# Kernel optimization log

Hardware: AMD Instinct MI355X
Metric: run time of the kernel (lower is better)

Reference implementation:

```python
import jax, jax.numpy as jnp
import numpy as np

VOCAB = 10000
HID = 256
BATCH = 32
STEPS = 256


def setup_inputs() -> dict:
    key = jax.random.key(0)
    k1, k2, k3, k4 = jax.random.split(key, 4)
    # glorot-uniform style scaling
    s_xh = np.sqrt(6.0 / (VOCAB + HID)).astype(np.float32)
    s_hh = np.sqrt(6.0 / (HID + HID)).astype(np.float32)
    s_d = np.sqrt(6.0 / (HID + VOCAB)).astype(np.float32)
    return {
        "tokens": jax.random.randint(k1, (BATCH, STEPS), 0, VOCAB, dtype=jnp.int32),
        "W_xh": jax.random.uniform(k2, (VOCAB, HID), jnp.float32, -s_xh, s_xh),
        "W_hh": jax.random.uniform(k3, (HID, HID), jnp.float32, -s_hh, s_hh),
        "b_h": jnp.zeros((HID,), jnp.float32),
        "W_d": jax.random.uniform(k4, (HID, VOCAB), jnp.float32, -s_d, s_d),
        "b_d": jnp.zeros((VOCAB,), jnp.float32),
        "h0": jnp.zeros((BATCH, HID), jnp.float32),
    }


def reference(tokens, W_xh, W_hh, b_h, W_d, b_d, h0):
    # call(): X = one_hot(transpose(tokens), vocab)  -> time-major [T, B, V]
    # one_hot(x) @ W_xh is exactly a row gather from W_xh (same math, efficient form)
    xw = W_xh[jnp.transpose(tokens)]  # [T, B, H]

    # SimpleRNNCell: h_t = tanh(x_t @ W_xh + h_{t-1} @ W_hh + b)
    def step(h, xt):
        h_new = jnp.tanh(xt + h @ W_hh + b_h)
        return h_new, h_new

    state, Y = jax.lax.scan(step, h0, xw)  # Y: [T, B, H], state: [B, H]

    # Dense over flattened sequence outputs -> [T*B, vocab]
    output = Y.reshape(-1, Y.shape[-1]) @ W_d + b_d
    return output, state
```

## Files before the change

kernel.cpp:

```cpp
#include <hip/hip_runtime.h>
#include <hip/hip_bf16.h>

#define VOCAB 10000
#define HID 256
#define BATCH 32
#define STEPS 256
#define MROWS (STEPS * BATCH)

typedef __bf16 bf16x8 __attribute__((ext_vector_type(8)));
typedef float f32x4 __attribute__((ext_vector_type(4)));

__global__ void transpose_wd_kernel(const float* __restrict__ Wd,
                                    __hip_bfloat16* __restrict__ WdT) {
    __shared__ __hip_bfloat16 tile[64][68];
    const int n0 = blockIdx.x * 64;
    const int k0 = blockIdx.y * 64;
    const int tid = threadIdx.x;
    const int lane = tid & 63;
    const int w = tid >> 6;

#pragma unroll
    for (int i = 0; i < 16; ++i) {
        int k = w * 16 + i;
        int n = lane;
        float v = (n0 + n < VOCAB) ? Wd[(size_t)(k0 + k) * VOCAB + n0 + n] : 0.f;
        tile[n][k] = __float2bfloat16(v);
    }
    __syncthreads();
#pragma unroll
    for (int i = 0; i < 16; ++i) {
        int n = w * 16 + i;
        int k = lane;
        if (n0 + n < VOCAB)
            WdT[(size_t)(n0 + n) * HID + k0 + k] = tile[n][k];
    }
}

#define HHALF 132

__global__ __launch_bounds__(512)
__attribute__((amdgpu_waves_per_eu(2, 2)))
void rnn_kernel(const int* __restrict__ tokens, const float* __restrict__ Wxh,
                const float* __restrict__ Whh, const float* __restrict__ bh,
                const float* __restrict__ h0, __hip_bfloat16* __restrict__ ybf,
                float* __restrict__ state_out) {
    const int b = blockIdx.x;
    const int tid = threadIdx.x;
    const int j = tid >> 1;
    const int q = tid & 1;

    __shared__ alignas(16) float hbuf[2][2][HHALF];

    float w[128];
#pragma unroll
    for (int i = 0; i < 128; ++i)
        w[i] = Whh[(size_t)(q * 128 + i) * HID + j];
#pragma unroll
    for (int i = 0; i < 128; ++i)
        asm volatile("" : "+v"(w[i]));

    if (q == 0) hbuf[0][j >> 7][j & 127] = h0[b * HID + j];
    const float bj = bh[j];
    const int* trow = tokens + b * STEPS;

    float x = Wxh[(size_t)trow[0] * HID + j];
    __syncthreads();

    float hn = 0.f;
    int cur = 0;
    for (int t = 0; t < STEPS; ++t) {
        int tn = (t + 1 < STEPS) ? t + 1 : t;
        float xn = Wxh[(size_t)trow[tn] * HID + j];

        const float* hrow = &hbuf[cur][q][0];
        float a0 = 0.f, a1 = 0.f, a2 = 0.f, a3 = 0.f;
#pragma unroll
        for (int i4 = 0; i4 < 32; ++i4) {
            float4 hv = *reinterpret_cast<const float4*>(&hrow[i4 * 4]);
            a0 += hv.x * w[i4 * 4 + 0];
            a1 += hv.y * w[i4 * 4 + 1];
            a2 += hv.z * w[i4 * 4 + 2];
            a3 += hv.w * w[i4 * 4 + 3];
        }
        float partial = (a0 + a1) + (a2 + a3);
        float sum = partial + __shfl_xor(partial, 1);

        float z = x + bj + sum;
        float e = __expf(2.f * z);
        hn = 1.f - 2.f / (e + 1.f);

        if (q == 0)
            hbuf[cur ^ 1][j >> 7][j & 127] = hn;
        else
            ybf[(size_t)t * (BATCH * HID) + b * HID + j] = __float2bfloat16(hn);

        __syncthreads();
        cur ^= 1;
        x = xn;
    }
    if (q == 0) state_out[b * HID + j] = hn;
}

__global__ void gemm_kernel(const __hip_bfloat16* __restrict__ A,
                            const __hip_bfloat16* __restrict__ BT,
                            const float* __restrict__ bd,
                            float* __restrict__ C) {
    const int n0 = blockIdx.x * 128;
    const int m0 = blockIdx.y * 128;
    const int tid = threadIdx.x;
    const int lane = tid & 63;
    const int wv = tid >> 6;
    const int wr = wv >> 1;
    const int wc = wv & 1;
    const int r15 = lane & 15;
    const int g = lane >> 4;

    __shared__ alignas(16) __hip_bfloat16 As[128][72];
    __shared__ alignas(16) __hip_bfloat16 Bs[128][72];

    f32x4 acc[4][4] = {};

    for (int kb = 0; kb < HID; kb += 64) {
        __syncthreads();
#pragma unroll
        for (int c = 0; c < 4; ++c) {
            int chunk = c * 256 + tid;
            int row = chunk >> 3;
            int cc = chunk & 7;
            bf16x8 av = *reinterpret_cast<const bf16x8*>(
                &A[(size_t)(m0 + row) * HID + kb + cc * 8]);
            *reinterpret_cast<bf16x8*>(&As[row][cc * 8]) = av;

            int nrow = n0 + row;
            bf16x8 bv;
#pragma unroll
            for (int e = 0; e < 8; ++e) bv[e] = (__bf16)0.f;
            if (nrow < VOCAB)
                bv = *reinterpret_cast<const bf16x8*>(
                    &BT[(size_t)nrow * HID + kb + cc * 8]);
            *reinterpret_cast<bf16x8*>(&Bs[row][cc * 8]) = bv;
        }
        __syncthreads();

#pragma unroll
        for (int kk = 0; kk < 64; kk += 32) {
            bf16x8 af[4], bfr[4];
#pragma unroll
            for (int m = 0; m < 4; ++m)
                af[m] = *reinterpret_cast<const bf16x8*>(
                    &As[wr * 64 + m * 16 + r15][kk + g * 8]);
#pragma unroll
            for (int n = 0; n < 4; ++n)
                bfr[n] = *reinterpret_cast<const bf16x8*>(
                    &Bs[wc * 64 + n * 16 + r15][kk + g * 8]);
#pragma unroll
            for (int m = 0; m < 4; ++m)
#pragma unroll
                for (int n = 0; n < 4; ++n)
                    acc[m][n] = __builtin_amdgcn_mfma_f32_16x16x32_bf16(
                        bfr[n], af[m], acc[m][n], 0, 0, 0);
        }
    }

#pragma unroll
    for (int m = 0; m < 4; ++m) {
        int row = m0 + wr * 64 + m * 16 + r15;
#pragma unroll
        for (int n = 0; n < 4; ++n) {
            int cb = n0 + wc * 64 + n * 16;
            if (cb + 15 < VOCAB) {
                int col = cb + g * 4;
                float4 bv = *reinterpret_cast<const float4*>(&bd[col]);
                f32x4 v = acc[m][n];
                v[0] += bv.x; v[1] += bv.y; v[2] += bv.z; v[3] += bv.w;
                *reinterpret_cast<f32x4*>(&C[(size_t)row * VOCAB + col]) = v;
            }
        }
    }
}

extern "C" void kernel_launch(void* const* d_in, const int* in_sizes, int n_in,
                              void* d_out, int out_size, void* d_ws, size_t ws_size,
                              hipStream_t stream) {
    const int* tokens  = (const int*)d_in[0];
    const float* Wxh   = (const float*)d_in[1];
    const float* Whh   = (const float*)d_in[2];
    const float* bh    = (const float*)d_in[3];
    const float* Wd    = (const float*)d_in[4];
    const float* bd    = (const float*)d_in[5];
    const float* h0    = (const float*)d_in[6];

    float* out = (float*)d_out;
    float* state_out = out + (size_t)MROWS * VOCAB;

    __hip_bfloat16* ybf = (__hip_bfloat16*)d_ws;
    __hip_bfloat16* wdt = (__hip_bfloat16*)((char*)d_ws + (size_t)MROWS * HID * 2);

    hipLaunchKernelGGL(transpose_wd_kernel, dim3(157, 4), dim3(256), 0, stream,
                       Wd, wdt);
    hipLaunchKernelGGL(rnn_kernel, dim3(BATCH), dim3(512), 0, stream,
                       tokens, Wxh, Whh, bh, h0, ybf, state_out);
    hipLaunchKernelGGL(gemm_kernel, dim3(79, 64), dim3(256), 0, stream,
                       ybf, wdt, bd, out);
}
```

Measured before the change: 351.2 us.

## Split RNN recurrence across eight lanes per column pair and restructure GEMM loads

The RNN kernel moves from 512 threads (two lanes per hidden unit, 128 weights each) to 1024 threads where each group of eight lanes computes two hidden units over 32-element K slices. Partial sums are reduced with DPP and ds_swizzle, which shortens the serial per-step dot product and the register footprint. The GEMM now loads the full 128x256 A tile into LDS once and streams B fragments directly from global memory with one-step register prefetch. The grid is also reordered so M varies fastest, letting blocks that share a W_d tile run together. The trade-offs are more synchronising threads per RNN step and uncached global B reads with larger LDS use in the GEMM.

Result: slower. 429.5 us (+22.3%).

```diff
diff --git a/kernel.cpp b/kernel.cpp
--- a/kernel.cpp
+++ b/kernel.cpp
@@ -9,6 +9,20 @@
 
 typedef __bf16 bf16x8 __attribute__((ext_vector_type(8)));
 typedef float f32x4 __attribute__((ext_vector_type(4)));
+
+template <int CTRL>
+static __device__ __forceinline__ float dpp_add(float s) {
+    int t = __builtin_amdgcn_update_dpp(
+        0, __builtin_bit_cast(int, s), CTRL, 0xf, 0xf, true);
+    return s + __builtin_bit_cast(float, t);
+}
+#define DPP_XOR1 0xB1
+#define DPP_XOR2 0x4E
+
+static __device__ __forceinline__ float swz4_add(float s) {
+    int t = __builtin_amdgcn_ds_swizzle(__builtin_bit_cast(int, s), 0x101F);
+    return s + __builtin_bit_cast(float, t);
+}
 
 __global__ void transpose_wd_kernel(const float* __restrict__ Wd,
                                     __hip_bfloat16* __restrict__ WdT) {
@@ -36,77 +50,105 @@
     }
 }
 
-#define HHALF 132
-
-__global__ __launch_bounds__(512)
-__attribute__((amdgpu_waves_per_eu(2, 2)))
+#define HSEG 36
+
+__global__ __launch_bounds__(1024)
+__attribute__((amdgpu_waves_per_eu(4, 4)))
 void rnn_kernel(const int* __restrict__ tokens, const float* __restrict__ Wxh,
                 const float* __restrict__ Whh, const float* __restrict__ bh,
                 const float* __restrict__ h0, __hip_bfloat16* __restrict__ ybf,
                 float* __restrict__ state_out) {
     const int b = blockIdx.x;
     const int tid = threadIdx.x;
-    const int j = tid >> 1;
-    const int q = tid & 1;
-
-    __shared__ alignas(16) float hbuf[2][2][HHALF];
-
-    float w[128];
-#pragma unroll
-    for (int i = 0; i < 128; ++i)
-        w[i] = Whh[(size_t)(q * 128 + i) * HID + j];
-#pragma unroll
-    for (int i = 0; i < 128; ++i)
-        asm volatile("" : "+v"(w[i]));
-
-    if (q == 0) hbuf[0][j >> 7][j & 127] = h0[b * HID + j];
-    const float bj = bh[j];
+    const int cg = tid >> 3;
+    const int q = tid & 7;
+    const int c0 = cg * 2;
+
+    __shared__ alignas(16) float hseg[2][8][HSEG];
+
+    float w0[32], w1[32];
+    {
+        const float* wp = Whh + (size_t)(q * 32) * HID + c0;
+#pragma unroll
+        for (int i = 0; i < 32; ++i) {
+            w0[i] = wp[(size_t)i * HID];
+            w1[i] = wp[(size_t)i * HID + 1];
+        }
+    }
+
+    const float bj0 = bh[c0];
+    const float bj1 = bh[c0 + 1];
     const int* trow = tokens + b * STEPS;
 
-    float x = Wxh[(size_t)trow[0] * HID + j];
+    if (q == 0) {
+        hseg[0][c0 >> 5][c0 & 31] = h0[b * HID + c0];
+        hseg[0][c0 >> 5][(c0 & 31) + 1] = h0[b * HID + c0 + 1];
+    }
+
+    float2 xv = *reinterpret_cast<const float2*>(&Wxh[(size_t)trow[0] * HID + c0]);
     __syncthreads();
 
-    float hn = 0.f;
+    float hn0 = 0.f, hn1 = 0.f;
     int cur = 0;
     for (int t = 0; t < STEPS; ++t) {
-        int tn = (t + 1 < STEPS) ? t + 1 : t;
-        float xn = Wxh[(size_t)trow[tn] * HID + j];
-
-        const float* hrow = &hbuf[cur][q][0];
-        float a0 = 0.f, a1 = 0.f, a2 = 0.f, a3 = 0.f;
-#pragma unroll
-        for (int i4 = 0; i4 < 32; ++i4) {
-            float4 hv = *reinterpret_cast<const float4*>(&hrow[i4 * 4]);
-            a0 += hv.x * w[i4 * 4 + 0];
-            a1 += hv.y * w[i4 * 4 + 1];
-            a2 += hv.z * w[i4 * 4 + 2];
-            a3 += hv.w * w[i4 * 4 + 3];
-        }
-        float partial = (a0 + a1) + (a2 + a3);
-        float sum = partial + __shfl_xor(partial, 1);
-
-        float z = x + bj + sum;
-        float e = __expf(2.f * z);
-        hn = 1.f - 2.f / (e + 1.f);
-
-        if (q == 0)
-            hbuf[cur ^ 1][j >> 7][j & 127] = hn;
-        else
-            ybf[(size_t)t * (BATCH * HID) + b * HID + j] = __float2bfloat16(hn);
+#pragma unroll
+        for (int i = 0; i < 32; ++i) {
+            asm volatile("" : "+v"(w0[i]), "+v"(w1[i]));
+        }
+
+        int ti = (t + 1 < STEPS) ? t + 1 : STEPS - 1;
+        float2 xn = *reinterpret_cast<const float2*>(
+            &Wxh[(size_t)trow[ti] * HID + c0]);
+
+        const float* hb = &hseg[cur][q][0];
+        float s0 = 0.f, s1 = 0.f;
+#pragma unroll
+        for (int j4 = 0; j4 < 8; ++j4) {
+            float4 hv = *reinterpret_cast<const float4*>(&hb[j4 * 4]);
+            s0 += hv.x * w0[j4 * 4 + 0] + hv.y * w0[j4 * 4 + 1] +
+                  hv.z * w0[j4 * 4 + 2] + hv.w * w0[j4 * 4 + 3];
+            s1 += hv.x * w1[j4 * 4 + 0] + hv.y * w1[j4 * 4 + 1] +
+                  hv.z * w1[j4 * 4 + 2] + hv.w * w1[j4 * 4 + 3];
+        }
+        s0 = dpp_add<DPP_XOR1>(s0);  s1 = dpp_add<DPP_XOR1>(s1);
+        s0 = dpp_add<DPP_XOR2>(s0);  s1 = dpp_add<DPP_XOR2>(s1);
+        s0 = swz4_add(s0);           s1 = swz4_add(s1);
+
+        float z0 = xv.x + bj0 + s0;
+        float z1 = xv.y + bj1 + s1;
+        float e0 = __expf(2.f * z0);
+        float e1 = __expf(2.f * z1);
+        hn0 = 1.f - 2.f / (e0 + 1.f);
+        hn1 = 1.f - 2.f / (e1 + 1.f);
+
+        if (q == 0) {
+            float2 hp = make_float2(hn0, hn1);
+            *reinterpret_cast<float2*>(&hseg[cur ^ 1][c0 >> 5][c0 & 31]) = hp;
+        } else if (q == 1) {
+            __hip_bfloat162 yp;
+            yp.x = __float2bfloat16(hn0);
+            yp.y = __float2bfloat16(hn1);
+            *reinterpret_cast<__hip_bfloat162*>(
+                &ybf[(size_t)t * (BATCH * HID) + b * HID + c0]) = yp;
+        }
 
         __syncthreads();
         cur ^= 1;
-        x = xn;
-    }
-    if (q == 0) state_out[b * HID + j] = hn;
-}
-
-__global__ void gemm_kernel(const __hip_bfloat16* __restrict__ A,
-                            const __hip_bfloat16* __restrict__ BT,
-                            const float* __restrict__ bd,
-                            float* __restrict__ C) {
-    const int n0 = blockIdx.x * 128;
-    const int m0 = blockIdx.y * 128;
+        xv = xn;
+    }
+    if (q == 1) {
+        state_out[b * HID + c0] = hn0;
+        state_out[b * HID + c0 + 1] = hn1;
+    }
+}
+
+__global__ __launch_bounds__(256)
+void gemm_kernel(const __hip_bfloat16* __restrict__ A,
+                 const __hip_bfloat16* __restrict__ BT,
+                 const float* __restrict__ bd,
+                 float* __restrict__ C) {
+    const int m0 = blockIdx.x * 128;
+    const int n0 = blockIdx.y * 128;
     const int tid = threadIdx.x;
     const int lane = tid & 63;
     const int wv = tid >> 6;
@@ -115,50 +157,62 @@
     const int r15 = lane & 15;
     const int g = lane >> 4;
 
-    __shared__ alignas(16) __hip_bfloat16 As[128][72];
-    __shared__ alignas(16) __hip_bfloat16 Bs[128][72];
+    __shared__ alignas(16) __hip_bfloat16 As[128][264];
+
+#pragma unroll
+    for (int c = 0; c < 16; ++c) {
+        int chunk = c * 256 + tid;
+        int row = chunk >> 5;
+        int cc = chunk & 31;
+        bf16x8 av = *reinterpret_cast<const bf16x8*>(
+            &A[(size_t)(m0 + row) * HID + cc * 8]);
+        *reinterpret_cast<bf16x8*>(&As[row][cc * 8]) = av;
+    }
+    __syncthreads();
+
+    const __hip_bfloat16* brow[4];
+    bool bok[4];
+#pragma unroll
+    for (int n = 0; n < 4; ++n) {
+        int rn = n0 + wc * 64 + n * 16 + r15;
+        bok[n] = rn < VOCAB;
+        brow[n] = BT + (size_t)(bok[n] ? rn : 0) * HID;
+    }
+    bf16x8 bzero;
+#pragma unroll
+    for (int e = 0; e < 8; ++e) bzero[e] = (__bf16)0.f;
 
     f32x4 acc[4][4] = {};
-
-    for (int kb = 0; kb < HID; kb += 64) {
-        __syncthreads();
-#pragma unroll
-        for (int c = 0; c < 4; ++c) {
-            int chunk = c * 256 + tid;
-            int row = chunk >> 3;
-            int cc = chunk & 7;
-            bf16x8 av = *reinterpret_cast<const bf16x8*>(
-                &A[(size_t)(m0 + row) * HID + kb + cc * 8]);
-            *reinterpret_cast<bf16x8*>(&As[row][cc * 8]) = av;
-
-            int nrow = n0 + row;
-            bf16x8 bv;
-#pragma unroll
-            for (int e = 0; e < 8; ++e) bv[e] = (__bf16)0.f;
-            if (nrow < VOCAB)
-                bv = *reinterpret_cast<const bf16x8*>(
-                    &BT[(size_t)nrow * HID + kb + cc * 8]);
-            *reinterpret_cast<bf16x8*>(&Bs[row][cc * 8]) = bv;
-        }
-        __syncthreads();
-
-#pragma unroll
-        for (int kk = 0; kk < 64; kk += 32) {
-            bf16x8 af[4], bfr[4];
-#pragma unroll
-            for (int m = 0; m < 4; ++m)
-                af[m] = *reinterpret_cast<const bf16x8*>(
-                    &As[wr * 64 + m * 16 + r15][kk + g * 8]);
+    bf16x8 bcur[4];
+#pragma unroll
+    for (int n = 0; n < 4; ++n)
+        bcur[n] = bok[n] ? *reinterpret_cast<const bf16x8*>(&brow[n][g * 8])
+                         : bzero;
+
+    for (int kk8 = 0; kk8 < 8; ++kk8) {
+        bf16x8 bnext[4];
+        if (kk8 < 7) {
+            int off = (kk8 + 1) * 32 + g * 8;
 #pragma unroll
             for (int n = 0; n < 4; ++n)
-                bfr[n] = *reinterpret_cast<const bf16x8*>(
-                    &Bs[wc * 64 + n * 16 + r15][kk + g * 8]);
-#pragma unroll
-            for (int m = 0; m < 4; ++m)
-#pragma unroll
-                for (int n = 0; n < 4; ++n)
-                    acc[m][n] = __builtin_amdgcn_mfma_f32_16x16x32_bf16(
-                        bfr[n], af[m], acc[m][n], 0, 0, 0);
+                bnext[n] = bok[n]
+                    ? *reinterpret_cast<const bf16x8*>(&brow[n][off])
+                    : bzero;
+        }
+        bf16x8 af[4];
+#pragma unroll
+        for (int m = 0; m < 4; ++m)
+            af[m] = *reinterpret_cast<const bf16x8*>(
+                &As[wr * 64 + m * 16 + r15][kk8 * 32 + g * 8]);
+#pragma unroll
+        for (int m = 0; m < 4; ++m)
+#pragma unroll
+            for (int n = 0; n < 4; ++n)
+                acc[m][n] = __builtin_amdgcn_mfma_f32_16x16x32_bf16(
+                    bcur[n], af[m], acc[m][n], 0, 0, 0);
+        if (kk8 < 7) {
+#pragma unroll
+            for (int n = 0; n < 4; ++n) bcur[n] = bnext[n];
         }
     }
 
@@ -198,8 +252,8 @@
 
     hipLaunchKernelGGL(transpose_wd_kernel, dim3(157, 4), dim3(256), 0, stream,
                        Wd, wdt);
-    hipLaunchKernelGGL(rnn_kernel, dim3(BATCH), dim3(512), 0, stream,
+    hipLaunchKernelGGL(rnn_kernel, dim3(BATCH), dim3(1024), 0, stream,
                        tokens, Wxh, Whh, bh, h0, ybf, state_out);
-    hipLaunchKernelGGL(gemm_kernel, dim3(79, 64), dim3(256), 0, stream,
+    hipLaunchKernelGGL(gemm_kernel, dim3(64, 79), dim3(256), 0, stream,
                        ybf, wdt, bd, out);
 }
```
